# Kernel tuning notes

Measured on AMD Instinct MI355X. Metric: run time of the kernel, lower is better.

The kernel has to match this reference:

```python
import jax, jax.numpy as jnp
import numpy as np

B, T, D_EMBED, HEAD = 8, 4096, 128, 64


def setup_inputs() -> dict:
    key = jax.random.key(0)
    k1, k2, k3, k4 = jax.random.split(key, 4)
    x = jax.random.normal(k1, (B, T, D_EMBED), dtype=jnp.float32)
    # torch nn.Linear(d_embed, head_size, bias=False): y = x @ W^T, W:[head,in].
    # We store W already transposed as [in, head] for x @ W.
    Wq = jax.random.normal(k2, (D_EMBED, HEAD), dtype=jnp.float32) * (1.0 / np.sqrt(D_EMBED))
    Wk = jax.random.normal(k3, (D_EMBED, HEAD), dtype=jnp.float32) * (1.0 / np.sqrt(D_EMBED))
    Wv = jax.random.normal(k4, (D_EMBED, HEAD), dtype=jnp.float32) * (1.0 / np.sqrt(D_EMBED))
    return {"x": x, "Wq": Wq, "Wk": Wk, "Wv": Wv}


def reference(x, Wq, Wk, Wv):
    # x: [B, T, D]; projections to [B, T, H]
    T_ = x.shape[1]
    D_ = x.shape[2]
    Q = x @ Wq
    K = x @ Wk
    V = x @ Wv
    # NOTE: source divides by sqrt(feature_dimension) == sqrt(d_embed), not head_size
    scores = jnp.einsum('bqh,bkh->bqk', Q, K) / jnp.sqrt(jnp.float32(D_))
    causal = jnp.tril(jnp.ones((T_, T_), dtype=bool))  # [T, T]
    scores = jnp.where(causal[None, :, :], scores, -jnp.inf)
    probs = jax.nn.softmax(scores, axis=-1)  # [B, T, T]
    return jnp.einsum('bqk,bkh->bqh', probs, V)
```

## Files before the change

### kernel.cpp

```cpp
#include <hip/hip_runtime.h>
#include <hip/hip_bf16.h>

typedef __attribute__((ext_vector_type(8))) short bf16x8;
typedef __attribute__((ext_vector_type(4))) short short4v;
typedef __attribute__((ext_vector_type(4))) float f32x4;

#define MFMA16(a, b, c) __builtin_amdgcn_mfma_f32_16x16x32_bf16((a), (b), (c), 0, 0, 0)

constexpr int Bn = 8, Tn = 4096, Dn = 128, Hn = 64;

__device__ inline unsigned short f2b(float f) {
    union { float f; unsigned u; } v; v.f = f;
    unsigned r = v.u + 0x7fff + ((v.u >> 16) & 1);
    return (unsigned short)(r >> 16);
}

__global__ void wtrans(const float* __restrict__ Wq,
                       const float* __restrict__ Wk,
                       const float* __restrict__ Wv,
                       unsigned short* __restrict__ WT) {
    int m = blockIdx.x;
    const float* W = (m == 0) ? Wq : (m == 1) ? Wk : Wv;
    unsigned short* o = WT + m * Hn * Dn;
    for (int i = threadIdx.x; i < Hn * Dn; i += blockDim.x) {
        int n = i >> 7, k = i & 127;
        o[i] = f2b(W[k * Hn + n]);
    }
}

__global__ __launch_bounds__(256) void qkv(const float* __restrict__ X,
                                           const unsigned short* __restrict__ WT,
                                           unsigned short* __restrict__ Qp,
                                           unsigned short* __restrict__ Kp,
                                           unsigned short* __restrict__ VTp) {
    __shared__ unsigned short xt[64 * 136];
    __shared__ unsigned short ot[64 * 72];
    int tid = threadIdx.x, w = tid >> 6, lane = tid & 63, quad = lane >> 4, l15 = lane & 15;
    int m0 = blockIdx.x * 64;
    int b = m0 >> 12, tloc = m0 & (Tn - 1);
    const float kLog2Scale = 0.12751879523175464f;

    #pragma unroll
    for (int c = 0; c < 8; c++) {
        int e = tid * 4 + c * 1024;
        int row = e >> 7, col = e & 127;
        f32x4 v = *(const f32x4*)&X[(size_t)(m0 + row) * Dn + col];
        short4v s4;
        s4[0] = (short)f2b(v[0]); s4[1] = (short)f2b(v[1]);
        s4[2] = (short)f2b(v[2]); s4[3] = (short)f2b(v[3]);
        *(short4v*)&xt[row * 136 + col] = s4;
    }
    __syncthreads();

    bf16x8 a[4];
    #pragma unroll
    for (int kt = 0; kt < 4; kt++)
        a[kt] = *(const bf16x8*)&xt[(w * 16 + l15) * 136 + kt * 32 + quad * 8];

    for (int mat = 0; mat < 3; mat++) {
        f32x4 acc[4];
        #pragma unroll
        for (int nt = 0; nt < 4; nt++) {
            acc[nt] = (f32x4){0.f, 0.f, 0.f, 0.f};
            const unsigned short* wtm = WT + mat * Hn * Dn + (size_t)(nt * 16 + l15) * Dn + quad * 8;
            #pragma unroll
            for (int kt = 0; kt < 4; kt++)
                acc[nt] = MFMA16(a[kt], *(const bf16x8*)&wtm[kt * 32], acc[nt]);
        }
        __syncthreads();
        if (mat < 2) {
            float sc = (mat == 0) ? kLog2Scale : 1.0f;
            #pragma unroll
            for (int nt = 0; nt < 4; nt++)
                #pragma unroll
                for (int rg = 0; rg < 4; rg++)
                    ot[(w * 16 + quad * 4 + rg) * 72 + nt * 16 + l15] = f2b(acc[nt][rg] * sc);
        } else {
            #pragma unroll
            for (int nt = 0; nt < 4; nt++) {
                short4v pk;
                pk[0] = (short)f2b(acc[nt][0]); pk[1] = (short)f2b(acc[nt][1]);
                pk[2] = (short)f2b(acc[nt][2]); pk[3] = (short)f2b(acc[nt][3]);
                *(short4v*)&ot[(nt * 16 + l15) * 72 + w * 16 + quad * 4] = pk;
            }
        }
        __syncthreads();
        if (mat < 2) {
            unsigned short* O = mat ? Kp : Qp;
            #pragma unroll
            for (int i = 0; i < 2; i++) {
                int row = (tid >> 3) + 32 * i, ch = tid & 7;
                *(bf16x8*)&O[(size_t)(m0 + row) * Hn + ch * 8] = *(const bf16x8*)&ot[row * 72 + ch * 8];
            }
        } else {
            #pragma unroll
            for (int i = 0; i < 2; i++) {
                int h = (tid >> 3) + 32 * i, ch = tid & 7;
                *(bf16x8*)&VTp[((size_t)(b * Hn + h)) * Tn + tloc + ch * 8] = *(const bf16x8*)&ot[h * 72 + ch * 8];
            }
        }
    }
}

__global__ __launch_bounds__(256) void attn(const unsigned short* __restrict__ Qp,
                                            const unsigned short* __restrict__ Kp,
                                            const unsigned short* __restrict__ VTp,
                                            float* __restrict__ Out) {
    __shared__ unsigned short Ps[4][32 * 40];
    __shared__ float Cbuf[2][32][66];
    __shared__ float Lbuf[2][64];

    int idx = blockIdx.x;
    int b = idx & 7;
    int j = (idx >> 3) & 31;
    int qt = (idx >> 8) ? j : (63 - j);

    int tid = threadIdx.x, w = tid >> 6, lane = tid & 63, quad = lane >> 4, l15 = lane & 15;
    int qh = w & 1, kh = w >> 1;

    int Q0 = qt * 64;
    const unsigned short* Kb = Kp + (size_t)b * Tn * Hn;
    const unsigned short* Vb = VTp + (size_t)b * Hn * Tn;

    f32x4 o[2][4];
    #pragma unroll
    for (int nq = 0; nq < 2; nq++)
        #pragma unroll
        for (int nh = 0; nh < 4; nh++) o[nq][nh] = (f32x4){0.f, 0.f, 0.f, 0.f};
    float li[2] = {0.f, 0.f};
    unsigned short* Pw = &Ps[w][0];

    bf16x8 kf0[2][2], vf0[4], kf1[2][2], vf1[4];
    {
        int kk = kh * 32;
        #pragma unroll
        for (int mt = 0; mt < 2; mt++)
            #pragma unroll
            for (int hc = 0; hc < 2; hc++)
                kf0[mt][hc] = *(const bf16x8*)&Kb[(size_t)(kk + mt * 16 + l15) * Hn + hc * 32 + quad * 8];
        #pragma unroll
        for (int nh = 0; nh < 4; nh++)
            vf0[nh] = *(const bf16x8*)&Vb[(size_t)(nh * 16 + l15) * Tn + kk + quad * 8];
    }
    bf16x8 qf[2][2];
    {
        const unsigned short* Qb = Qp + ((size_t)b * Tn + Q0 + qh * 32) * Hn;
        #pragma unroll
        for (int nq = 0; nq < 2; nq++)
            #pragma unroll
            for (int hc = 0; hc < 2; hc++)
                qf[nq][hc] = *(const bf16x8*)&Qb[(nq * 16 + l15) * Hn + hc * 32 + quad * 8];
    }

    auto body = [&](bf16x8 (&kc)[2][2], bf16x8 (&vc)[4],
                    bf16x8 (&kn)[2][2], bf16x8 (&vn)[4], int kt) {
        if (kt < qt) {
            int kk2 = (kt + 1) * 64 + kh * 32;
            #pragma unroll
            for (int mt = 0; mt < 2; mt++)
                #pragma unroll
                for (int hc = 0; hc < 2; hc++)
                    kn[mt][hc] = *(const bf16x8*)&Kb[(size_t)(kk2 + mt * 16 + l15) * Hn + hc * 32 + quad * 8];
            #pragma unroll
            for (int nh = 0; nh < 4; nh++)
                vn[nh] = *(const bf16x8*)&Vb[(size_t)(nh * 16 + l15) * Tn + kk2 + quad * 8];
        }
        int kk = kt * 64 + kh * 32;
        f32x4 s[2][2];
        #pragma unroll
        for (int mt = 0; mt < 2; mt++)
            #pragma unroll
            for (int nq = 0; nq < 2; nq++) {
                f32x4 acc = {0.f, 0.f, 0.f, 0.f};
                acc = MFMA16(kc[mt][0], qf[nq][0], acc);
                acc = MFMA16(kc[mt][1], qf[nq][1], acc);
                s[mt][nq] = acc;
            }
        bool diag = (kt == qt);
        int kbase = kk + quad * 4;
        int qbase = Q0 + qh * 32 + l15;
        #pragma unroll
        for (int mt = 0; mt < 2; mt++) {
            #pragma unroll
            for (int nq = 0; nq < 2; nq++) {
                short4v pk;
                #pragma unroll
                for (int rg = 0; rg < 4; rg++) {
                    float p = __builtin_amdgcn_exp2f(s[mt][nq][rg]);
                    if (diag && (kbase + mt * 16 + rg > qbase + nq * 16)) p = 0.f;
                    li[nq] += p;
                    pk[rg] = (short)f2b(p);
                }
                *(short4v*)&Pw[(nq * 16 + l15) * 40 + mt * 16 + quad * 4] = pk;
            }
        }
        bf16x8 pf[2];
        #pragma unroll
        for (int nq = 0; nq < 2; nq++)
            pf[nq] = *(const bf16x8*)&Pw[(nq * 16 + l15) * 40 + quad * 8];
        #pragma unroll
        for (int nq = 0; nq < 2; nq++)
            #pragma unroll
            for (int nh = 0; nh < 4; nh++)
                o[nq][nh] = MFMA16(pf[nq], vc[nh], o[nq][nh]);
    };

    int kt = 0;
    for (;;) {
        body(kf0, vf0, kf1, vf1, kt);
        if (++kt > qt) break;
        body(kf1, vf1, kf0, vf0, kt);
        if (++kt > qt) break;
    }

    __syncthreads();
    #pragma unroll
    for (int nq = 0; nq < 2; nq++) {
        li[nq] += __shfl_xor(li[nq], 16);
        li[nq] += __shfl_xor(li[nq], 32);
    }
    if (lane < 16) {
        Lbuf[kh][qh * 32 + lane]      = li[0];
        Lbuf[kh][qh * 32 + 16 + lane] = li[1];
    }
    if (kh == 1) {
        #pragma unroll
        for (int nq = 0; nq < 2; nq++)
            #pragma unroll
            for (int nh = 0; nh < 4; nh++)
                #pragma unroll
                for (int rg = 0; rg < 4; rg++)
                    Cbuf[qh][nq * 16 + quad * 4 + rg][nh * 16 + l15] = o[nq][nh][rg];
    }
    __syncthreads();
    if (kh == 0) {
        #pragma unroll
        for (int nq = 0; nq < 2; nq++) {
            #pragma unroll
            for (int rg = 0; rg < 4; rg++) {
                int qloc = nq * 16 + quad * 4 + rg;
                float lt = Lbuf[0][qh * 32 + qloc] + Lbuf[1][qh * 32 + qloc];
                float inv = 1.0f / lt;
                size_t row = (size_t)b * Tn + Q0 + qh * 32 + qloc;
                #pragma unroll
                for (int nh = 0; nh < 4; nh++) {
                    float val = o[nq][nh][rg] + Cbuf[qh][qloc][nh * 16 + l15];
                    Out[row * Hn + nh * 16 + l15] = val * inv;
                }
            }
        }
    }
}

extern "C" void kernel_launch(void* const* d_in, const int* in_sizes, int n_in,
                              void* d_out, int out_size, void* d_ws, size_t ws_size,
                              hipStream_t stream) {
    const float* X  = (const float*)d_in[0];
    const float* Wq = (const float*)d_in[1];
    const float* Wk = (const float*)d_in[2];
    const float* Wv = (const float*)d_in[3];
    float* out = (float*)d_out;

    char* ws = (char*)d_ws;
    size_t szQ = (size_t)Bn * Tn * Hn * sizeof(unsigned short);
    unsigned short* Qp  = (unsigned short*)(ws);
    unsigned short* Kp  = (unsigned short*)(ws + szQ);
    unsigned short* VTp = (unsigned short*)(ws + 2 * szQ);
    unsigned short* WT  = (unsigned short*)(ws + 3 * szQ);

    wtrans<<<3, 256, 0, stream>>>(Wq, Wk, Wv, WT);
    qkv<<<Bn * Tn / 64, 256, 0, stream>>>(X, WT, Qp, Kp, VTp);
    attn<<<Bn * Tn / 64, 256, 0, stream>>>(Qp, Kp, VTp, out);
}
```

Measured before the change: 153.1 us.

## Split causal attention KV range across blocks with atomic accumulation and normalize pass

```diff
diff --git a/kernel.cpp b/kernel.cpp
--- a/kernel.cpp
+++ b/kernel.cpp
@@ -105,15 +105,22 @@
 __global__ __launch_bounds__(256) void attn(const unsigned short* __restrict__ Qp,
                                             const unsigned short* __restrict__ Kp,
                                             const unsigned short* __restrict__ VTp,
-                                            float* __restrict__ Out) {
+                                            float* __restrict__ OutAcc,
+                                            float* __restrict__ Lsum) {
     __shared__ unsigned short Ps[4][32 * 40];
     __shared__ float Cbuf[2][32][66];
     __shared__ float Lbuf[2][64];
 
     int idx = blockIdx.x;
     int b = idx & 7;
-    int j = (idx >> 3) & 31;
-    int qt = (idx >> 8) ? j : (63 - j);
+    int c = 159 - (idx >> 3);
+    int qt, ch;
+    if (c < 16)      { qt = c;                ch = 0; }
+    else if (c < 48) { int t = c - 16; qt = 16 + (t >> 1); ch = t & 1; }
+    else if (c < 96) { int t = c - 48; int q3 = t / 3; qt = 32 + q3; ch = t - 3 * q3; }
+    else             { int t = c - 96; qt = 48 + (t >> 2); ch = t & 3; }
+    int k0 = ch * 16;
+    int k1 = min(qt, k0 + 15);
 
     int tid = threadIdx.x, w = tid >> 6, lane = tid & 63, quad = lane >> 4, l15 = lane & 15;
     int qh = w & 1, kh = w >> 1;
@@ -132,7 +139,7 @@
 
     bf16x8 kf0[2][2], vf0[4], kf1[2][2], vf1[4];
     {
-        int kk = kh * 32;
+        int kk = k0 * 64 + kh * 32;
         #pragma unroll
         for (int mt = 0; mt < 2; mt++)
             #pragma unroll
@@ -154,7 +161,7 @@
 
     auto body = [&](bf16x8 (&kc)[2][2], bf16x8 (&vc)[4],
                     bf16x8 (&kn)[2][2], bf16x8 (&vn)[4], int kt) {
-        if (kt < qt) {
+        if (kt < k1) {
             int kk2 = (kt + 1) * 64 + kh * 32;
             #pragma unroll
             for (int mt = 0; mt < 2; mt++)
@@ -205,12 +212,12 @@
                 o[nq][nh] = MFMA16(pf[nq], vc[nh], o[nq][nh]);
     };
 
-    int kt = 0;
+    int kt = k0;
     for (;;) {
         body(kf0, vf0, kf1, vf1, kt);
-        if (++kt > qt) break;
+        if (++kt > k1) break;
         body(kf1, vf1, kf0, vf0, kt);
-        if (++kt > qt) break;
+        if (++kt > k1) break;
     }
 
     __syncthreads();
@@ -239,17 +246,25 @@
             #pragma unroll
             for (int rg = 0; rg < 4; rg++) {
                 int qloc = nq * 16 + quad * 4 + rg;
-                float lt = Lbuf[0][qh * 32 + qloc] + Lbuf[1][qh * 32 + qloc];
-                float inv = 1.0f / lt;
                 size_t row = (size_t)b * Tn + Q0 + qh * 32 + qloc;
                 #pragma unroll
-                for (int nh = 0; nh < 4; nh++) {
-                    float val = o[nq][nh][rg] + Cbuf[qh][qloc][nh * 16 + l15];
-                    Out[row * Hn + nh * 16 + l15] = val * inv;
-                }
-            }
-        }
-    }
+                for (int nh = 0; nh < 4; nh++)
+                    atomicAdd(&OutAcc[row * Hn + nh * 16 + l15],
+                              o[nq][nh][rg] + Cbuf[qh][qloc][nh * 16 + l15]);
+            }
+        }
+    }
+    if (w == 0)
+        atomicAdd(&Lsum[(size_t)b * Tn + Q0 + lane], Lbuf[0][lane] + Lbuf[1][lane]);
+}
+
+__global__ __launch_bounds__(256) void norm_out(float* __restrict__ Out,
+                                                const float* __restrict__ Lsum) {
+    int i = (blockIdx.x * 256 + threadIdx.x) * 4;
+    f32x4 v = *(const f32x4*)&Out[i];
+    float inv = 1.0f / Lsum[i >> 6];
+    v[0] *= inv; v[1] *= inv; v[2] *= inv; v[3] *= inv;
+    *(f32x4*)&Out[i] = v;
 }
 
 extern "C" void kernel_launch(void* const* d_in, const int* in_sizes, int n_in,
@@ -267,8 +282,12 @@
     unsigned short* Kp  = (unsigned short*)(ws + szQ);
     unsigned short* VTp = (unsigned short*)(ws + 2 * szQ);
     unsigned short* WT  = (unsigned short*)(ws + 3 * szQ);
-
+    float*          Ls  = (float*)(ws + 3 * szQ + 64 * 1024);
+
+    hipMemsetAsync(out, 0, (size_t)out_size * sizeof(float), stream);
+    hipMemsetAsync(Ls, 0, (size_t)Bn * Tn * sizeof(float), stream);
     wtrans<<<3, 256, 0, stream>>>(Wq, Wk, Wv, WT);
     qkv<<<Bn * Tn / 64, 256, 0, stream>>>(X, WT, Qp, Kp, VTp);
-    attn<<<Bn * Tn / 64, 256, 0, stream>>>(Qp, Kp, VTp, out);
-}
+    attn<<<1280, 256, 0, stream>>>(Qp, Kp, VTp, out, Ls);
+    norm_out<<<(Bn * Tn * Hn / 4) / 256, 256, 0, stream>>>(out, Ls);
+}
```

After: 178.4 us. 16.5% more time.
